# Kernel optimization log

Measured on AMD Instinct MI355X. Metric: run time of the kernel, lower is better.

## Reference

```python
import jax, jax.numpy as jnp
import numpy as np
import math
from jax import lax

D = 256      # d_model
H = 8        # heads
DK = D // H  # 32
P = 16       # patch size
IMG = 224
S = (IMG // P) ** 2 + 1  # 197
B = 64
EPS = 1e-5


def _ln(x, g, b):
    m = jnp.mean(x, axis=-1, keepdims=True)
    v = jnp.mean((x - m) ** 2, axis=-1, keepdims=True)
    return (x - m) / jnp.sqrt(v + EPS) * g + b


def _attn(q_in, k_in, v_in, wq, bq, wk, bk, wv, bv, wo, bo, mask):
    # torch Linear: y = x @ W^T + b
    def heads(x, w, b):
        y = x @ w.T + b
        bsz, s, _ = y.shape
        return y.reshape(bsz, s, H, DK).transpose(0, 2, 1, 3)  # [b,h,s,dk]
    q = heads(q_in, wq, bq)
    k = heads(k_in, wk, bk)
    v = heads(v_in, wv, bv)
    att = jnp.einsum('bhqd,bhkd->bhqk', q, k) / math.sqrt(DK)
    if mask is not None:
        att = jnp.where(mask == 0, -jnp.inf, att)
    att = jax.nn.softmax(att, axis=-1)
    o = jnp.einsum('bhqk,bhkd->bhqd', att, v)
    bsz, s, _ = q_in.shape  # output reshape uses q's shape (faithful to source)
    o = o.transpose(0, 2, 1, 3).reshape(bsz, s, D)
    return o @ wo.T + bo


def _patch_embed(img, conv_w, conv_b, cls, pos):
    x = lax.conv_general_dilated(img, conv_w, window_strides=(P, P),
                                 padding='VALID',
                                 dimension_numbers=('NCHW', 'OIHW', 'NCHW'))
    x = x + conv_b[None, :, None, None]
    bsz = img.shape[0]
    x = x.reshape(bsz, D, -1).transpose(0, 2, 1)  # [B,196,D]
    cls_t = jnp.broadcast_to(cls, (bsz, 1, D))
    x = jnp.concatenate([x, cls_t], axis=1)  # cls appended at END (faithful)
    return x + pos


def setup_inputs() -> dict:
    key = jax.random.key(0)
    ks = iter(jax.random.split(key, 64))
    nrm = lambda shape, s=0.02: jax.random.normal(next(ks), shape, jnp.float32) * s
    inp = {
        'enc_out': jax.random.normal(next(ks), (B, 3, IMG, IMG), jnp.float32),
        'dec_in': jax.random.normal(next(ks), (B, S, D), jnp.float32),
        'mask': jnp.ones((1, 1, S, S), jnp.int32),
        'conv_w': nrm((D, 3, P, P)),
        'conv_b': jnp.zeros((D,), jnp.float32),
        'cls': nrm((1, 1, D), 1.0),
        'pos': nrm((1, S, D), 1.0),
        'ff_w1': nrm((4 * D, D)), 'ff_b1': jnp.zeros((4 * D,), jnp.float32),
        'ff_w2': nrm((D, 4 * D)), 'ff_b2': jnp.zeros((D,), jnp.float32),
        'ln1_g': jnp.ones((D,), jnp.float32), 'ln1_b': jnp.zeros((D,), jnp.float32),
        'ln2_g': jnp.ones((D,), jnp.float32), 'ln2_b': jnp.zeros((D,), jnp.float32),
        'ln3_g': jnp.ones((D,), jnp.float32), 'ln3_b': jnp.zeros((D,), jnp.float32),
    }
    for p in ('a1', 'a2'):
        for n in ('wq', 'wk', 'wv', 'wo'):
            inp[f'{p}_{n}'] = nrm((D, D))
            inp[f'{p}_b{n[1]}'] = jnp.zeros((D,), jnp.float32)
    return inp


def reference(enc_out, dec_in, mask, conv_w, conv_b, cls, pos,
              ff_w1, ff_b1, ff_w2, ff_b2,
              ln1_g, ln1_b, ln2_g, ln2_b, ln3_g, ln3_b,
              a1_wq, a1_bq, a1_wk, a1_bk, a1_wv, a1_bv, a1_wo, a1_bo,
              a2_wq, a2_bq, a2_wk, a2_bk, a2_wv, a2_bv, a2_wo, a2_bo):
    e = _patch_embed(enc_out, conv_w, conv_b, cls, pos)  # [B,197,D]
    x = dec_in
    x = _ln(x + _attn(dec_in, dec_in, dec_in,
                      a1_wq, a1_bq, a1_wk, a1_bk, a1_wv, a1_bv, a1_wo, a1_bo,
                      None), ln1_g, ln1_b)
    # faithful: q=k=enc_out, v=dec_in, with mask
    x = _ln(x + _attn(e, e, dec_in,
                      a2_wq, a2_bq, a2_wk, a2_bk, a2_wv, a2_bv, a2_wo, a2_bo,
                      mask), ln2_g, ln2_b)
    ff = jax.nn.relu(x @ ff_w1.T + ff_b1) @ ff_w2.T + ff_b2
    x = _ln(x + ff, ln3_g, ln3_b)
    return x
```

## Files before the change

### kernel.cpp

```cpp
#include <hip/hip_runtime.h>
#include <hip/hip_bf16.h>
#include <math.h>

#define DMODEL 256
#define NH 8
#define DKH 32
#define SEQ 197
#define BATCH 64
#define NPAT 196
#define FFDIM 1024
#define KCONV 768
#define EPSLN 1e-5f
#define MROWS (BATCH * SEQ)
#define SP 224

typedef __attribute__((ext_vector_type(8))) short short8;
typedef __attribute__((ext_vector_type(4))) short short4v;
typedef __attribute__((ext_vector_type(4))) float floatx4;

__device__ inline short f2b(float f) {
  unsigned u = __float_as_uint(f);
  unsigned r = (u + 0x7FFFu + ((u >> 16) & 1u)) >> 16;
  return (short)r;
}
__device__ inline float b2f(short s) {
  return __uint_as_float(((unsigned)(unsigned short)s) << 16);
}

typedef const __attribute__((address_space(1))) unsigned int gu32;
typedef __attribute__((address_space(3))) unsigned int lu32;
__device__ __forceinline__ void gl_lds16(const void* g, void* l) {
  __builtin_amdgcn_global_load_lds((gu32*)g, (lu32*)l, 16, 0, 0);
}

__device__ __forceinline__ void gemm64_body(
    char* smem, int bx, int by,
    const short* __restrict__ A, const short* __restrict__ W,
    const float* __restrict__ bias, const short* __restrict__ resb,
    float* __restrict__ outf, short* __restrict__ outb,
    int N, int K, int relu)
{
  short* Al = (short*)smem;
  short* Bl = (short*)(smem + 16384);
  const int t = threadIdx.x;
  const int wave = t >> 6, lane = t & 63;
  const int wm = (wave & 1) * 32, wn = (wave >> 1) * 32;
  const int ml = lane & 15, quad = lane >> 4;
  const int m7 = ml & 7;
  const int m0 = bx * 64, n0 = by * 64;

  const int rs = t >> 3;
  const int cs = (t & 7) ^ (rs & 7);
  const short* gA0 = A + (size_t)(m0 + rs) * K + cs * 8;
  const short* gA1 = A + (size_t)(m0 + rs + 32) * K + cs * 8;
  const short* gB0 = W + (size_t)(n0 + rs) * K + cs * 8;
  const short* gB1 = W + (size_t)(n0 + rs + 32) * K + cs * 8;

  int offA[2][2], offB[2][2];
#pragma unroll
  for (int kk = 0; kk < 2; kk++)
#pragma unroll
    for (int i = 0; i < 2; i++) {
      int ra = wm + i * 16 + ml;
      offA[kk][i] = ra * 64 + (((kk * 4 + quad) ^ m7) * 8);
      int rb = wn + i * 16 + ml;
      offB[kk][i] = rb * 64 + (((kk * 4 + quad) ^ m7) * 8);
    }

  floatx4 z = {0.f, 0.f, 0.f, 0.f};
  floatx4 acc[2][2] = {{z, z}, {z, z}};

  const int niter = K >> 6;
  gl_lds16(gA0, Al + t * 8);
  gl_lds16(gA1, Al + t * 8 + 2048);
  gl_lds16(gB0, Bl + t * 8);
  gl_lds16(gB1, Bl + t * 8 + 2048);
  for (int k = 0; k < niter; k++) {
    int cur = k & 1;
    if (k + 1 < niter) {
      int nb = (cur ^ 1) * 4096;
      int k0 = (k + 1) << 6;
      gl_lds16(gA0 + k0, Al + nb + t * 8);
      gl_lds16(gA1 + k0, Al + nb + t * 8 + 2048);
      gl_lds16(gB0 + k0, Bl + nb + t * 8);
      gl_lds16(gB1 + k0, Bl + nb + t * 8 + 2048);
      __builtin_amdgcn_s_waitcnt(0x0F74);
    } else {
      __builtin_amdgcn_s_waitcnt(0x0F70);
    }
    __asm__ volatile("s_barrier" ::: "memory");
    const short* Ac = Al + cur * 4096;
    const short* Bc = Bl + cur * 4096;
#pragma unroll
    for (int kk = 0; kk < 2; kk++) {
      short8 a0 = *(const short8*)&Ac[offA[kk][0]];
      short8 a1 = *(const short8*)&Ac[offA[kk][1]];
      short8 b0 = *(const short8*)&Bc[offB[kk][0]];
      short8 b1 = *(const short8*)&Bc[offB[kk][1]];
      acc[0][0] = __builtin_amdgcn_mfma_f32_16x16x32_bf16(a0, b0, acc[0][0], 0, 0, 0);
      acc[0][1] = __builtin_amdgcn_mfma_f32_16x16x32_bf16(a0, b1, acc[0][1], 0, 0, 0);
      acc[1][0] = __builtin_amdgcn_mfma_f32_16x16x32_bf16(a1, b0, acc[1][0], 0, 0, 0);
      acc[1][1] = __builtin_amdgcn_mfma_f32_16x16x32_bf16(a1, b1, acc[1][1], 0, 0, 0);
    }
    __asm__ volatile("s_barrier" ::: "memory");
  }
#pragma unroll
  for (int i = 0; i < 2; i++)
#pragma unroll
    for (int j = 0; j < 2; j++)
#pragma unroll
      for (int rr = 0; rr < 4; rr++) {
        int row = m0 + wm + i * 16 + quad * 4 + rr;
        int col = n0 + wn + j * 16 + ml;
        float v = acc[i][j][rr] + bias[col];
        if (resb) v += b2f(resb[(size_t)row * N + col]);
        if (relu) v = fmaxf(v, 0.f);
        if (outf) outf[(size_t)row * N + col] = v;
        if (outb) outb[(size_t)row * N + col] = f2b(v);
      }
}

__device__ __forceinline__ void conv64_body(
    char* smem, int bx, int by,
    const float* __restrict__ img, const short* __restrict__ W,
    const float* __restrict__ cb, const float* __restrict__ pos,
    short* __restrict__ e)
{
  short* Al = (short*)smem;
  short* Bl = (short*)(smem + 8192);
  const int t = threadIdx.x;
  const int wave = t >> 6, lane = t & 63;
  const int wm = (wave & 1) * 32, wn = (wave >> 1) * 32;
  const int ml = lane & 15, quad = lane >> 4;
  const int m7 = ml & 7;
  const int m0 = bx * 64, n0 = by * 64;

  int rA = t >> 3, cg = t & 7;
  int pr_off = cg >> 1;
  int px_off = (cg & 1) * 8;
  int csw = cg ^ (rA & 7);
  const float* baseA[2];
  short* lA[2];
#pragma unroll
  for (int p = 0; p < 2; p++) {
    int m = m0 + rA + p * 32;
    int b = m / NPAT, pp = m - b * NPAT;
    int py = pp / 14, px = pp - py * 14;
    baseA[p] = img + (size_t)b * 3 * 50176 + (size_t)(py * 16) * 224 + px * 16 + px_off;
    lA[p] = &Al[(rA + p * 32) * 64 + csw * 8];
  }
  int rs = t >> 3;
  int cs = (t & 7) ^ (rs & 7);
  const short* gB0 = W + (size_t)(n0 + rs) * KCONV + cs * 8;
  const short* gB1 = W + (size_t)(n0 + rs + 32) * KCONV + cs * 8;

  int offA[2][2], offB[2][2];
#pragma unroll
  for (int kk = 0; kk < 2; kk++)
#pragma unroll
    for (int i = 0; i < 2; i++) {
      int ra = wm + i * 16 + ml;
      offA[kk][i] = ra * 64 + (((kk * 4 + quad) ^ m7) * 8);
      int rb = wn + i * 16 + ml;
      offB[kk][i] = rb * 64 + (((kk * 4 + quad) ^ m7) * 8);
    }

  floatx4 z = {0.f, 0.f, 0.f, 0.f};
  floatx4 acc[2][2] = {{z, z}, {z, z}};

  for (int k0 = 0; k0 < KCONV; k0 += 64) {
    int ch = k0 >> 8;
    int rr0 = (k0 & 255) >> 4;
    __syncthreads();
    gl_lds16(gB0 + k0, Bl + t * 8);
    gl_lds16(gB1 + k0, Bl + t * 8 + 2048);
#pragma unroll
    for (int p = 0; p < 2; p++) {
      const float* ap = baseA[p] + (size_t)ch * 50176 + (rr0 + pr_off) * 224;
      float4 a0 = *(const float4*)ap;
      float4 a1 = *(const float4*)(ap + 4);
      short8 av;
      av[0] = f2b(a0.x); av[1] = f2b(a0.y); av[2] = f2b(a0.z); av[3] = f2b(a0.w);
      av[4] = f2b(a1.x); av[5] = f2b(a1.y); av[6] = f2b(a1.z); av[7] = f2b(a1.w);
      *(short8*)lA[p] = av;
    }
    __builtin_amdgcn_s_waitcnt(0x0F70);
    __syncthreads();
#pragma unroll
    for (int kk = 0; kk < 2; kk++) {
      short8 a0 = *(const short8*)&Al[offA[kk][0]];
      short8 a1 = *(const short8*)&Al[offA[kk][1]];
      short8 b0 = *(const short8*)&Bl[offB[kk][0]];
      short8 b1 = *(const short8*)&Bl[offB[kk][1]];
      acc[0][0] = __builtin_amdgcn_mfma_f32_16x16x32_bf16(a0, b0, acc[0][0], 0, 0, 0);
      acc[0][1] = __builtin_amdgcn_mfma_f32_16x16x32_bf16(a0, b1, acc[0][1], 0, 0, 0);
      acc[1][0] = __builtin_amdgcn_mfma_f32_16x16x32_bf16(a1, b0, acc[1][0], 0, 0, 0);
      acc[1][1] = __builtin_amdgcn_mfma_f32_16x16x32_bf16(a1, b1, acc[1][1], 0, 0, 0);
    }
  }
#pragma unroll
  for (int i = 0; i < 2; i++)
#pragma unroll
    for (int j = 0; j < 2; j++)
#pragma unroll
      for (int rr = 0; rr < 4; rr++) {
        int mrow = m0 + wm + i * 16 + quad * 4 + rr;
        int b2 = mrow / NPAT, p2 = mrow - b2 * NPAT;
        int col = n0 + wn + j * 16 + ml;
        e[((size_t)b2 * SEQ + p2) * DMODEL + col] =
            f2b(acc[i][j][rr] + cb[col] + pos[p2 * DMODEL + col]);
      }
}

__device__ __forceinline__ void attn_body(
    char* smem, int bid2,
    const short* __restrict__ qp, int qstr,
    const short* __restrict__ kp, int kstr,
    const short* __restrict__ vp, int vstr,
    const unsigned long long* __restrict__ mbits,
    short* __restrict__ op)
{
  short (*ks)[40] = (short(*)[40])smem;
  short (*vt)[SP + 8] = (short(*)[SP + 8])(smem + 17920);
  short* psw = (short*)(smem + 32768);
  int bh = bid2 >> 1, half = bid2 & 1;
  int b = bh >> 3, h = bh & 7;
  int t = threadIdx.x;
  int wave = t >> 6, lane = t & 63;
  int ml = lane & 15, quad = lane >> 4;
  short* ps = psw + wave * 640;

  const short* kb = kp + (size_t)b * SEQ * kstr + h * DKH;
  const short* vb = vp + (size_t)b * SEQ * vstr + h * DKH;
  for (int idx = t; idx < SEQ * 4; idx += 256) {
    int s = idx >> 2, c = (idx & 3) * 8;
    *(short8*)&ks[s][c] = *(const short8*)(kb + (size_t)s * kstr + c);
  }
  for (int idx = t; idx < SEQ * 4; idx += 256) {
    int s = idx >> 2, c = (idx & 3) * 8;
    short8 v8 = *(const short8*)(vb + (size_t)s * vstr + c);
#pragma unroll
    for (int j = 0; j < 8; j++) vt[c + j][s] = v8[j];
  }
  for (int idx = t; idx < DKH * (SP - SEQ); idx += 256) {
    int d = idx / (SP - SEQ), j = SEQ + idx - d * (SP - SEQ);
    vt[d][j] = 0;
  }
  __syncthreads();

  const float scale = 0.17677669529663687f;
  floatx4 z = {0.f, 0.f, 0.f, 0.f};

  for (int tt = 0; tt < 2; tt++) {
    int ti = half * 8 + wave * 2 + tt;
    int q0 = ti * 16;
    if (q0 >= SEQ) continue;
    int qrow = q0 + ml;
    int qc = qrow < SEQ ? qrow : SEQ - 1;
    short8 qf = *(const short8*)(qp + ((size_t)b * SEQ + qc) * qstr + h * DKH + quad * 8);
    const unsigned long long* mrow = mbits + (size_t)qc * 4;

    floatx4 accO0 = z, accO1 = z;
    float mrun = -1e30f, lrun = 0.f;

    for (int st = 0; st < 7; st++) {
      int j0 = st * 32;
      short8 k0 = *(const short8*)&ks[j0 + ml][quad * 8];
      short8 k1 = *(const short8*)&ks[j0 + 16 + ml][quad * 8];
      floatx4 s0 = __builtin_amdgcn_mfma_f32_16x16x32_bf16(k0, qf, z, 0, 0, 0);
      floatx4 s1 = __builtin_amdgcn_mfma_f32_16x16x32_bf16(k1, qf, z, 0, 0, 0);
      unsigned long long mb = mrow[j0 >> 6] >> (j0 & 63);
      float sv[8];
#pragma unroll
      for (int r = 0; r < 4; r++) {
        int jl = quad * 4 + r;
        sv[r]     = ((mb >> jl) & 1ull)        ? s0[r] * scale : -1e38f;
        sv[4 + r] = ((mb >> (16 + jl)) & 1ull) ? s1[r] * scale : -1e38f;
      }
      float tm = sv[0];
#pragma unroll
      for (int i = 1; i < 8; i++) tm = fmaxf(tm, sv[i]);
      tm = fmaxf(tm, __shfl_xor(tm, 16));
      tm = fmaxf(tm, __shfl_xor(tm, 32));
      float nm = fmaxf(mrun, tm);
      float alpha = __expf(mrun - nm);
      float pv[8];
      float psum = 0.f;
#pragma unroll
      for (int i = 0; i < 8; i++) { pv[i] = __expf(sv[i] - nm); psum += pv[i]; }
      psum += __shfl_xor(psum, 16);
      psum += __shfl_xor(psum, 32);
      lrun = lrun * alpha + psum;
      mrun = nm;
      accO0 = accO0 * alpha;
      accO1 = accO1 * alpha;
      short4v p0, p1;
#pragma unroll
      for (int r = 0; r < 4; r++) { p0[r] = f2b(pv[r]); p1[r] = f2b(pv[4 + r]); }
      *(short4v*)&ps[ml * 40 + quad * 4]      = p0;
      *(short4v*)&ps[ml * 40 + 16 + quad * 4] = p1;
      __asm__ volatile("s_waitcnt lgkmcnt(0)" ::: "memory");
      short8 pf = *(const short8*)&ps[ml * 40 + quad * 8];
      short8 vf0 = *(const short8*)&vt[ml][j0 + quad * 8];
      short8 vf1 = *(const short8*)&vt[16 + ml][j0 + quad * 8];
      accO0 = __builtin_amdgcn_mfma_f32_16x16x32_bf16(vf0, pf, accO0, 0, 0, 0);
      accO1 = __builtin_amdgcn_mfma_f32_16x16x32_bf16(vf1, pf, accO1, 0, 0, 0);
    }
    if (qrow < SEQ) {
      float inv = 1.f / lrun;
      short* ob = op + ((size_t)b * SEQ + qrow) * DMODEL + h * DKH;
      short4v o0, o1;
#pragma unroll
      for (int r = 0; r < 4; r++) {
        o0[r] = f2b(accO0[r] * inv);
        o1[r] = f2b(accO1[r] * inv);
      }
      *(short4v*)(ob + quad * 4)      = o0;
      *(short4v*)(ob + 16 + quad * 4) = o1;
    }
  }
}

__global__ __launch_bounds__(256) void phase0(
    const float* wq1, const float* wk1, const float* wv1,
    const float* bq1, const float* bk1, const float* bv1,
    const float* wq2, const float* wk2, const float* bq2, const float* bk2,
    const float* wv2s, const float* wo1, const float* wo2,
    const float* ffw1, const float* ffw2, const float* convw,
    short* Wqkv1, float* Bqkv1, short* Wqk2, float* Bqk2,
    short* Wv2, short* Wo1, short* Wo2, short* Wff1, short* Wff2, short* Wconv,
    const int* mask, unsigned long long* bits, unsigned long long* ones,
    const float* cls, const float* pos, short* e,
    const float* dec, short* dec_bf)
{
  int bid = blockIdx.x;
  int t = threadIdx.x;
  if (bid < 1024) {
    int i = bid * 256 + t;
    if (i < 65536) {
      Wqkv1[i] = f2b(wq1[i]); Wqkv1[65536 + i] = f2b(wk1[i]); Wqkv1[131072 + i] = f2b(wv1[i]);
      Wqk2[i] = f2b(wq2[i]);  Wqk2[65536 + i] = f2b(wk2[i]);
      Wv2[i] = f2b(wv2s[i]);  Wo1[i] = f2b(wo1[i]);  Wo2[i] = f2b(wo2[i]);
    }
    Wff1[i] = f2b(ffw1[i]); Wff2[i] = f2b(ffw2[i]);
    if (i < 196608) Wconv[i] = f2b(convw[i]);
    if (i < 256) {
      Bqkv1[i] = bq1[i]; Bqkv1[256 + i] = bk1[i]; Bqkv1[512 + i] = bv1[i];
      Bqk2[i] = bq2[i];  Bqk2[256 + i] = bk2[i];
    }
  } else if (bid < 1028) {
    int idx = (bid - 1024) * 256 + t;
    if (idx < SEQ * 4) {
      int r = idx >> 2, w = idx & 3;
      unsigned long long bb = 0ull, oo = 0ull;
      for (int j = 0; j < 64; j++) {
        int c = w * 64 + j;
        if (c < SEQ) {
          oo |= (1ull << j);
          if (mask[r * SEQ + c] != 0) bb |= (1ull << j);
        }
      }
      bits[idx] = bb;
      ones[idx] = oo;
    }
  } else if (bid < 1092) {
    int b = bid - 1028, d = t;
    e[((size_t)b * SEQ + NPAT) * DMODEL + d] = f2b(cls[d] + pos[NPAT * DMODEL + d]);
  } else {
    const int ND = (MROWS * DMODEL) / 8;
    int i = (bid - 1092) * 256 + t;
    if (i < ND) {
      float4 a0 = ((const float4*)dec)[i * 2];
      float4 a1 = ((const float4*)dec)[i * 2 + 1];
      short8 o;
      o[0] = f2b(a0.x); o[1] = f2b(a0.y); o[2] = f2b(a0.z); o[3] = f2b(a0.w);
      o[4] = f2b(a1.x); o[5] = f2b(a1.y); o[6] = f2b(a1.z); o[7] = f2b(a1.w);
      ((short8*)dec_bf)[i] = o;
    }
  }
}

__global__ __launch_bounds__(256) void phase1(
    const float* __restrict__ enc, const short* __restrict__ Wconv,
    const float* __restrict__ conv_b, const float* __restrict__ pos,
    short* __restrict__ e_bf,
    const short* __restrict__ dec_bf,
    const short* __restrict__ Wqkv1, const float* __restrict__ Bqkv1,
    short* __restrict__ qkv1,
    const short* __restrict__ Wv2, const float* __restrict__ bv2,
    short* __restrict__ v2)
{
  __shared__ char smem[32768];
  int bid = blockIdx.x;
  if (bid < 784) {
    conv64_body(smem, bid % 196, bid / 196, enc, Wconv, conv_b, pos, e_bf);
  } else if (bid < 3148) {
    int idx = bid - 784;
    gemm64_body(smem, idx % 197, idx / 197, dec_bf, Wqkv1, Bqkv1, nullptr,
                nullptr, qkv1, 768, 256, 0);
  } else {
    int idx = bid - 3148;
    gemm64_body(smem, idx % 197, idx / 197, dec_bf, Wv2, bv2, nullptr,
                nullptr, v2, 256, 256, 0);
  }
}

__global__ __launch_bounds__(256) void phase2(
    const short* __restrict__ qkv1, const unsigned long long* __restrict__ mones,
    short* __restrict__ o1,
    const short* __restrict__ e_bf, const short* __restrict__ Wqk2,
    const float* __restrict__ Bqk2, short* __restrict__ qk2)
{
  __shared__ char smem[37888];
  int bid = blockIdx.x;
  if (bid < 1024) {
    attn_body(smem, bid, qkv1, 768, qkv1 + 256, 768, qkv1 + 512, 768, mones, o1);
  } else {
    int idx = bid - 1024;
    gemm64_body(smem, idx % 197, idx / 197, e_bf, Wqk2, Bqk2, nullptr,
                nullptr, qk2, 512, 256, 0);
  }
}

__global__ __launch_bounds__(256) void phase3(
    const short* __restrict__ o1, const short* __restrict__ Wo1,
    const float* __restrict__ bo1, const short* __restrict__ dec_bf,
    short* __restrict__ t_bf,
    const short* __restrict__ qk2, const short* __restrict__ v2,
    const unsigned long long* __restrict__ mbits, short* __restrict__ o2)
{
  __shared__ char smem[37888];
  int bid = blockIdx.x;
  if (bid < 788) {
    gemm64_body(smem, bid % 197, bid / 197, o1, Wo1, bo1, dec_bf,
                nullptr, t_bf, 256, 256, 0);
  } else {
    attn_body(smem, bid - 788, qk2, 512, qk2 + 256, 512, v2, 256, mbits, o2);
  }
}

__global__ __launch_bounds__(256) void gemm_k(
    const short* __restrict__ A, const short* __restrict__ W,
    const float* __restrict__ bias, const short* __restrict__ resb,
    float* __restrict__ outf, short* __restrict__ outb, int N, int K, int relu)
{
  __shared__ char smem[32768];
  gemm64_body(smem, blockIdx.x, blockIdx.y, A, W, bias, resb, outf, outb, N, K, relu);
}

__global__ __launch_bounds__(256) void ln_bf(
    const short* __restrict__ x, const float* __restrict__ g,
    const float* __restrict__ bt, float* __restrict__ outf,
    short* __restrict__ outb)
{
  int wave = threadIdx.x >> 6, lane = threadIdx.x & 63;
  int row = blockIdx.x * 4 + wave;
  short4v xv = *(const short4v*)(x + (size_t)row * DMODEL + lane * 4);
  float v0 = b2f(xv[0]), v1 = b2f(xv[1]), v2 = b2f(xv[2]), v3 = b2f(xv[3]);
  float s = v0 + v1 + v2 + v3;
  for (int off = 32; off; off >>= 1) s += __shfl_down(s, off);
  s = __shfl(s, 0);
  float mean = s * (1.0f / DMODEL);
  float d0 = v0 - mean, d1 = v1 - mean, d2 = v2 - mean, d3 = v3 - mean;
  float vv = d0 * d0 + d1 * d1 + d2 * d2 + d3 * d3;
  for (int off = 32; off; off >>= 1) vv += __shfl_down(vv, off);
  vv = __shfl(vv, 0);
  float inv = rsqrtf(vv * (1.0f / DMODEL) + EPSLN);
  float4 gg = *(const float4*)(g + lane * 4);
  float4 bb = *(const float4*)(bt + lane * 4);
  float r0 = d0 * inv * gg.x + bb.x;
  float r1 = d1 * inv * gg.y + bb.y;
  float r2 = d2 * inv * gg.z + bb.z;
  float r3 = d3 * inv * gg.w + bb.w;
  if (outf) {
    float4 o = {r0, r1, r2, r3};
    *(float4*)(outf + (size_t)row * DMODEL + lane * 4) = o;
  }
  if (outb) {
    short4v o;
    o[0] = f2b(r0); o[1] = f2b(r1); o[2] = f2b(r2); o[3] = f2b(r3);
    *(short4v*)(outb + (size_t)row * DMODEL + lane * 4) = o;
  }
}

extern "C" void kernel_launch(void* const* d_in, const int* in_sizes, int n_in,
                              void* d_out, int out_size, void* d_ws, size_t ws_size,
                              hipStream_t stream)
{
  const float* enc    = (const float*)d_in[0];
  const float* dec_in = (const float*)d_in[1];
  const int*   mask   = (const int*)  d_in[2];
  const float* conv_w = (const float*)d_in[3];
  const float* conv_b = (const float*)d_in[4];
  const float* cls    = (const float*)d_in[5];
  const float* pos    = (const float*)d_in[6];
  const float* ff_w1  = (const float*)d_in[7];
  const float* ff_b1  = (const float*)d_in[8];
  const float* ff_w2  = (const float*)d_in[9];
  const float* ff_b2  = (const float*)d_in[10];
  const float* ln1_g  = (const float*)d_in[11];
  const float* ln1_b  = (const float*)d_in[12];
  const float* ln2_g  = (const float*)d_in[13];
  const float* ln2_b  = (const float*)d_in[14];
  const float* ln3_g  = (const float*)d_in[15];
  const float* ln3_b  = (const float*)d_in[16];
  const float* a1_wq = (const float*)d_in[17]; const float* a1_bq = (const float*)d_in[18];
  const float* a1_wk = (const float*)d_in[19]; const float* a1_bk = (const float*)d_in[20];
  const float* a1_wv = (const float*)d_in[21]; const float* a1_bv = (const float*)d_in[22];
  const float* a1_wo = (const float*)d_in[23]; const float* a1_bo = (const float*)d_in[24];
  const float* a2_wq = (const float*)d_in[25]; const float* a2_bq = (const float*)d_in[26];
  const float* a2_wk = (const float*)d_in[27]; const float* a2_bk = (const float*)d_in[28];
  const float* a2_wv = (const float*)d_in[29]; const float* a2_bv = (const float*)d_in[30];
  const float* a2_wo = (const float*)d_in[31]; const float* a2_bo = (const float*)d_in[32];

  char* wsB = (char*)d_ws;
  short* Wqkv1 = (short*)wsB;
  short* Wqk2  = Wqkv1 + 196608;
  short* Wv2   = Wqk2 + 131072;
  short* Wo1   = Wv2 + 65536;
  short* Wo2   = Wo1 + 65536;
  short* Wff1  = Wo2 + 65536;
  short* Wff2  = Wff1 + 262144;
  short* Wconv = Wff2 + 262144;
  float* Bqkv1 = (float*)(Wconv + 196608);
  float* Bqk2  = Bqkv1 + 768;
  unsigned long long* mbits = (unsigned long long*)(Bqk2 + 512);
  unsigned long long* mones = mbits + 788;

  const size_t MB = 1048576;
  short* dec_bf = (short*)(wsB + 3 * MB);
  short* e_bf   = (short*)(wsB + 10 * MB);
  short* qkv1   = (short*)(wsB + 17 * MB);
  short* o1     = (short*)(wsB + 37 * MB);
  short* qk2    = (short*)(wsB + 44 * MB);
  short* v2     = (short*)(wsB + 57 * MB);
  short* h_buf  = (short*)(wsB + 64 * MB);
  short* t_bf   = (short*)(wsB + 90 * MB);
  short* x1b    = (short*)(wsB + 97 * MB);
  short* x2b    = (short*)(wsB + 104 * MB);
  short* o2     = o1;

  dim3 blk(256);
  const int M = MROWS;

  phase0<<<2668, blk, 0, stream>>>(
      a1_wq, a1_wk, a1_wv, a1_bq, a1_bk, a1_bv,
      a2_wq, a2_wk, a2_bq, a2_bk, a2_wv, a1_wo, a2_wo,
      ff_w1, ff_w2, conv_w,
      Wqkv1, Bqkv1, Wqk2, Bqk2, Wv2, Wo1, Wo2, Wff1, Wff2, Wconv,
      mask, mbits, mones, cls, pos, e_bf, dec_in, dec_bf);

  phase1<<<3936, blk, 0, stream>>>(
      enc, Wconv, conv_b, pos, e_bf,
      dec_bf, Wqkv1, Bqkv1, qkv1, Wv2, a2_bv, v2);

  phase2<<<2600, blk, 0, stream>>>(
      qkv1, mones, o1, e_bf, Wqk2, Bqk2, qk2);

  phase3<<<1812, blk, 0, stream>>>(
      o1, Wo1, a1_bo, dec_bf, t_bf, qk2, v2, mbits, o2);

  ln_bf<<<M / 4, blk, 0, stream>>>(t_bf, ln1_g, ln1_b, nullptr, x1b);

  gemm_k<<<dim3(197, 4), blk, 0, stream>>>(
      o2, Wo2, a2_bo, x1b, nullptr, t_bf, 256, 256, 0);

  ln_bf<<<M / 4, blk, 0, stream>>>(t_bf, ln2_g, ln2_b, nullptr, x2b);

  gemm_k<<<dim3(197, 16), blk, 0, stream>>>(
      x2b, Wff1, ff_b1, nullptr, nullptr, h_buf, FFDIM, 256, 1);

  gemm_k<<<dim3(197, 4), blk, 0, stream>>>(
      h_buf, Wff2, ff_b2, x2b, nullptr, t_bf, 256, 1024, 0);

  ln_bf<<<M / 4, blk, 0, stream>>>(t_bf, ln3_g, ln3_b, (float*)d_out, nullptr);
}
```

Measured before the change: 333.8 us.

## Fuse LayerNorm into full-width GEMM epilogues and reorder block tile mapping

Adds a 64x256 full-row GEMM body whose epilogue applies bias, residual and LayerNorm within the block. This removes the three separate LayerNorm kernels and the bf16 intermediate round trip through t_bf. Phase3 now runs attention blocks first and the fused Wo1+LN1 blocks after. Block-to-tile mapping across phases is changed so consecutive blocks share the same A row tile. The cost is that the fused GEMMs launch only 197 blocks, which lowers parallelism and raises register pressure from 16 accumulator tiles.

```diff
diff --git a/kernel.cpp b/kernel.cpp
--- a/kernel.cpp
+++ b/kernel.cpp
@@ -120,6 +120,106 @@
       }
 }
 
+__device__ __forceinline__ void gemm_full_body(
+    char* smem, int bx,
+    const short* __restrict__ A, const short* __restrict__ W,
+    const float* __restrict__ bias, const short* __restrict__ resb,
+    const float* __restrict__ g, const float* __restrict__ bln,
+    short* __restrict__ outb, float* __restrict__ outfin, int K)
+{
+  short* Al = (short*)smem;
+  short* Bl = (short*)(smem + 8192);
+  const int t = threadIdx.x;
+  const int wave = t >> 6, lane = t & 63;
+  const int ml = lane & 15, quad = lane >> 4;
+  const int m0 = bx * 64;
+
+  const int rs = t >> 2;
+  const int cs = (t & 3) ^ (rs & 3);
+  const short* gA = A + (size_t)(m0 + rs) * K + cs * 8;
+  const short* gB[4];
+#pragma unroll
+  for (int j = 0; j < 4; j++)
+    gB[j] = W + (size_t)(j * 64 + rs) * K + cs * 8;
+
+  const int offA = (wave * 16 + ml) * 32 + ((quad ^ (ml & 3)) * 8);
+  const int offBb = ml * 32 + ((quad ^ (ml & 3)) * 8);
+
+  floatx4 zv = {0.f, 0.f, 0.f, 0.f};
+  floatx4 acc[16];
+#pragma unroll
+  for (int jj = 0; jj < 16; jj++) acc[jj] = zv;
+
+  const int niter = K >> 5;
+  gl_lds16(gA, Al + t * 8);
+#pragma unroll
+  for (int j = 0; j < 4; j++) gl_lds16(gB[j], Bl + j * 2048 + t * 8);
+  for (int k = 0; k < niter; k++) {
+    int cur = k & 1;
+    if (k + 1 < niter) {
+      int k0 = (k + 1) << 5;
+      int nbA = (cur ^ 1) * 2048, nbB = (cur ^ 1) * 8192;
+      gl_lds16(gA + k0, Al + nbA + t * 8);
+#pragma unroll
+      for (int j = 0; j < 4; j++) gl_lds16(gB[j] + k0, Bl + nbB + j * 2048 + t * 8);
+      __builtin_amdgcn_s_waitcnt(0x0F75);
+    } else {
+      __builtin_amdgcn_s_waitcnt(0x0F70);
+    }
+    __asm__ volatile("s_barrier" ::: "memory");
+    const short* Ac = Al + cur * 2048;
+    const short* Bc = Bl + cur * 8192;
+    short8 a = *(const short8*)&Ac[offA];
+#pragma unroll
+    for (int jj = 0; jj < 16; jj++) {
+      short8 b = *(const short8*)&Bc[offBb + jj * 512];
+      acc[jj] = __builtin_amdgcn_mfma_f32_16x16x32_bf16(a, b, acc[jj], 0, 0, 0);
+    }
+    __asm__ volatile("s_barrier" ::: "memory");
+  }
+
+  const int rbase = m0 + wave * 16 + quad * 4;
+  float bias_r[16], g_r[16], bl_r[16];
+#pragma unroll
+  for (int jj = 0; jj < 16; jj++) {
+    int c = jj * 16 + ml;
+    bias_r[jj] = bias[c];
+    g_r[jj] = g[c];
+    bl_r[jj] = bln[c];
+  }
+#pragma unroll
+  for (int jj = 0; jj < 16; jj++)
+#pragma unroll
+    for (int rr = 0; rr < 4; rr++)
+      acc[jj][rr] += bias_r[jj] + b2f(resb[(size_t)(rbase + rr) * DMODEL + jj * 16 + ml]);
+#pragma unroll
+  for (int rr = 0; rr < 4; rr++) {
+    float s = 0.f;
+#pragma unroll
+    for (int jj = 0; jj < 16; jj++) s += acc[jj][rr];
+    s += __shfl_xor(s, 1); s += __shfl_xor(s, 2);
+    s += __shfl_xor(s, 4); s += __shfl_xor(s, 8);
+    float mean = s * (1.0f / DMODEL);
+    float vs = 0.f;
+#pragma unroll
+    for (int jj = 0; jj < 16; jj++) {
+      float d = acc[jj][rr] - mean;
+      vs += d * d;
+    }
+    vs += __shfl_xor(vs, 1); vs += __shfl_xor(vs, 2);
+    vs += __shfl_xor(vs, 4); vs += __shfl_xor(vs, 8);
+    float inv = rsqrtf(vs * (1.0f / DMODEL) + EPSLN);
+    int row = rbase + rr;
+#pragma unroll
+    for (int jj = 0; jj < 16; jj++) {
+      float o = (acc[jj][rr] - mean) * inv * g_r[jj] + bl_r[jj];
+      int col = jj * 16 + ml;
+      if (outb) outb[(size_t)row * DMODEL + col] = f2b(o);
+      if (outfin) outfin[(size_t)row * DMODEL + col] = o;
+    }
+  }
+}
+
 __device__ __forceinline__ void conv64_body(
     char* smem, int bx, int by,
     const float* __restrict__ img, const short* __restrict__ W,
@@ -393,14 +493,14 @@
   __shared__ char smem[32768];
   int bid = blockIdx.x;
   if (bid < 784) {
-    conv64_body(smem, bid % 196, bid / 196, enc, Wconv, conv_b, pos, e_bf);
+    conv64_body(smem, bid >> 2, bid & 3, enc, Wconv, conv_b, pos, e_bf);
   } else if (bid < 3148) {
     int idx = bid - 784;
-    gemm64_body(smem, idx % 197, idx / 197, dec_bf, Wqkv1, Bqkv1, nullptr,
+    gemm64_body(smem, idx / 12, idx % 12, dec_bf, Wqkv1, Bqkv1, nullptr,
                 nullptr, qkv1, 768, 256, 0);
   } else {
     int idx = bid - 3148;
-    gemm64_body(smem, idx % 197, idx / 197, dec_bf, Wv2, bv2, nullptr,
+    gemm64_body(smem, idx >> 2, idx & 3, dec_bf, Wv2, bv2, nullptr,
                 nullptr, v2, 256, 256, 0);
   }
 }
@@ -417,70 +517,48 @@
     attn_body(smem, bid, qkv1, 768, qkv1 + 256, 768, qkv1 + 512, 768, mones, o1);
   } else {
     int idx = bid - 1024;
-    gemm64_body(smem, idx % 197, idx / 197, e_bf, Wqk2, Bqk2, nullptr,
+    gemm64_body(smem, idx >> 3, idx & 7, e_bf, Wqk2, Bqk2, nullptr,
                 nullptr, qk2, 512, 256, 0);
   }
 }
 
 __global__ __launch_bounds__(256) void phase3(
+    const short* __restrict__ qk2, const short* __restrict__ v2,
+    const unsigned long long* __restrict__ mbits, short* __restrict__ o2,
     const short* __restrict__ o1, const short* __restrict__ Wo1,
     const float* __restrict__ bo1, const short* __restrict__ dec_bf,
-    short* __restrict__ t_bf,
-    const short* __restrict__ qk2, const short* __restrict__ v2,
-    const unsigned long long* __restrict__ mbits, short* __restrict__ o2)
-{
-  __shared__ char smem[37888];
+    const float* __restrict__ ln1_g, const float* __restrict__ ln1_b,
+    short* __restrict__ x1b)
+{
+  __shared__ char smem[40960];
   int bid = blockIdx.x;
-  if (bid < 788) {
-    gemm64_body(smem, bid % 197, bid / 197, o1, Wo1, bo1, dec_bf,
-                nullptr, t_bf, 256, 256, 0);
+  if (bid < 1024) {
+    attn_body(smem, bid, qk2, 512, qk2 + 256, 512, v2, 256, mbits, o2);
   } else {
-    attn_body(smem, bid - 788, qk2, 512, qk2 + 256, 512, v2, 256, mbits, o2);
-  }
+    gemm_full_body(smem, bid - 1024, o1, Wo1, bo1, dec_bf, ln1_g, ln1_b,
+                   x1b, nullptr, 256);
+  }
+}
+
+__global__ __launch_bounds__(256) void gemm_full_k(
+    const short* __restrict__ A, const short* __restrict__ W,
+    const float* __restrict__ bias, const short* __restrict__ resb,
+    const float* __restrict__ g, const float* __restrict__ bln,
+    short* __restrict__ outb, float* __restrict__ outfin, int K)
+{
+  __shared__ char smem[40960];
+  gemm_full_body(smem, blockIdx.x, A, W, bias, resb, g, bln, outb, outfin, K);
 }
 
 __global__ __launch_bounds__(256) void gemm_k(
     const short* __restrict__ A, const short* __restrict__ W,
     const float* __restrict__ bias, const short* __restrict__ resb,
-    float* __restrict__ outf, short* __restrict__ outb, int N, int K, int relu)
+    float* __restrict__ outf, short* __restrict__ outb,
+    int N, int K, int relu, int nby)
 {
   __shared__ char smem[32768];
-  gemm64_body(smem, blockIdx.x, blockIdx.y, A, W, bias, resb, outf, outb, N, K, relu);
-}
-
-__global__ __launch_bounds__(256) void ln_bf(
-    const short* __restrict__ x, const float* __restrict__ g,
-    const float* __restrict__ bt, float* __restrict__ outf,
-    short* __restrict__ outb)
-{
-  int wave = threadIdx.x >> 6, lane = threadIdx.x & 63;
-  int row = blockIdx.x * 4 + wave;
-  short4v xv = *(const short4v*)(x + (size_t)row * DMODEL + lane * 4);
-  float v0 = b2f(xv[0]), v1 = b2f(xv[1]), v2 = b2f(xv[2]), v3 = b2f(xv[3]);
-  float s = v0 + v1 + v2 + v3;
-  for (int off = 32; off; off >>= 1) s += __shfl_down(s, off);
-  s = __shfl(s, 0);
-  float mean = s * (1.0f / DMODEL);
-  float d0 = v0 - mean, d1 = v1 - mean, d2 = v2 - mean, d3 = v3 - mean;
-  float vv = d0 * d0 + d1 * d1 + d2 * d2 + d3 * d3;
-  for (int off = 32; off; off >>= 1) vv += __shfl_down(vv, off);
-  vv = __shfl(vv, 0);
-  float inv = rsqrtf(vv * (1.0f / DMODEL) + EPSLN);
-  float4 gg = *(const float4*)(g + lane * 4);
-  float4 bb = *(const float4*)(bt + lane * 4);
-  float r0 = d0 * inv * gg.x + bb.x;
-  float r1 = d1 * inv * gg.y + bb.y;
-  float r2 = d2 * inv * gg.z + bb.z;
-  float r3 = d3 * inv * gg.w + bb.w;
-  if (outf) {
-    float4 o = {r0, r1, r2, r3};
-    *(float4*)(outf + (size_t)row * DMODEL + lane * 4) = o;
-  }
-  if (outb) {
-    short4v o;
-    o[0] = f2b(r0); o[1] = f2b(r1); o[2] = f2b(r2); o[3] = f2b(r3);
-    *(short4v*)(outb + (size_t)row * DMODEL + lane * 4) = o;
-  }
+  gemm64_body(smem, blockIdx.x / nby, blockIdx.x % nby, A, W, bias, resb,
+              outf, outb, N, K, relu);
 }
 
 extern "C" void kernel_launch(void* const* d_in, const int* in_sizes, int n_in,
@@ -535,13 +613,11 @@
   short* qk2    = (short*)(wsB + 44 * MB);
   short* v2     = (short*)(wsB + 57 * MB);
   short* h_buf  = (short*)(wsB + 64 * MB);
-  short* t_bf   = (short*)(wsB + 90 * MB);
   short* x1b    = (short*)(wsB + 97 * MB);
   short* x2b    = (short*)(wsB + 104 * MB);
   short* o2     = o1;
 
   dim3 blk(256);
-  const int M = MROWS;
 
   phase0<<<2668, blk, 0, stream>>>(
       a1_wq, a1_wk, a1_wv, a1_bq, a1_bk, a1_bv,
@@ -557,21 +633,15 @@
   phase2<<<2600, blk, 0, stream>>>(
       qkv1, mones, o1, e_bf, Wqk2, Bqk2, qk2);
 
-  phase3<<<1812, blk, 0, stream>>>(
-      o1, Wo1, a1_bo, dec_bf, t_bf, qk2, v2, mbits, o2);
-
-  ln_bf<<<M / 4, blk, 0, stream>>>(t_bf, ln1_g, ln1_b, nullptr, x1b);
-
-  gemm_k<<<dim3(197, 4), blk, 0, stream>>>(
-      o2, Wo2, a2_bo, x1b, nullptr, t_bf, 256, 256, 0);
-
-  ln_bf<<<M / 4, blk, 0, stream>>>(t_bf, ln2_g, ln2_b, nullptr, x2b);
-
-  gemm_k<<<dim3(197, 16), blk, 0, stream>>>(
-      x2b, Wff1, ff_b1, nullptr, nullptr, h_buf, FFDIM, 256, 1);
-
-  gemm_k<<<dim3(197, 4), blk, 0, stream>>>(
-      h_buf, Wff2, ff_b2, x2b, nullptr, t_bf, 256, 1024, 0);
-
-  ln_bf<<<M / 4, blk, 0, stream>>>(t_bf, ln3_g, ln3_b, (float*)d_out, nullptr);
-}
+  phase3<<<1221, blk, 0, stream>>>(
+      qk2, v2, mbits, o2, o1, Wo1, a1_bo, dec_bf, ln1_g, ln1_b, x1b);
+
+  gemm_full_k<<<197, blk, 0, stream>>>(
+      o2, Wo2, a2_bo, x1b, ln2_g, ln2_b, x2b, nullptr, 256);
+
+  gemm_k<<<3152, blk, 0, stream>>>(
+      x2b, Wff1, ff_b1, nullptr, nullptr, h_buf, FFDIM, 256, 1, 16);
+
+  gemm_full_k<<<197, blk, 0, stream>>>(
+      h_buf, Wff2, ff_b2, x2b, ln3_g, ln3_b, nullptr, (float*)d_out, 1024);
+}
```

Result: no change. 338.8 us (+1.5%).
